# Kernel optimization log

Measured on AMD Instinct MI355X. Metric: run time of the kernel, lower is better.

## Reference

```python
import jax, jax.numpy as jnp
import numpy as np

ALPHA_MIN = 1e-6
SN_EPS = 1e-6


def _spectral_normalize(W, u):
    # One power iteration (torch spectral_norm, n_power_iterations=1).
    v = W.T @ u
    v = v / (jnp.linalg.norm(v) + SN_EPS)
    u1 = W @ v
    u1 = u1 / (jnp.linalg.norm(u1) + SN_EPS)
    u1 = jax.lax.stop_gradient(u1)
    v = jax.lax.stop_gradient(v)
    sigma = u1 @ (W @ v)
    return W / sigma


def setup_inputs() -> dict:
    key = jax.random.key(0)
    ks = jax.random.split(key, 11)
    B, T, D, K = 32, 2048, 512, 128
    x = jax.random.normal(ks[0], (B, T, D), jnp.float32)
    dt = jax.random.uniform(ks[1], (B, T), jnp.float32)
    alpha_mod = jax.random.normal(ks[2], (B, T, K), jnp.float32)
    omega_mod = jax.random.normal(ks[3], (B, T, K), jnp.float32)
    tau_mod = jax.random.normal(ks[4], (B, T, 1), jnp.float32)
    s_real_raw = jax.random.normal(ks[5], (K,), jnp.float32)
    s_imag = jax.random.normal(ks[6], (K,), jnp.float32)
    tau_raw = jax.random.normal(ks[7], (1,), jnp.float32)
    W_orig = jax.random.normal(ks[8], (K, D), jnp.float32) * (1.0 / np.sqrt(D))
    b = jax.random.normal(ks[9], (K,), jnp.float32) * 0.01
    u_sn = jax.random.normal(ks[10], (K,), jnp.float32)
    u_sn = u_sn / jnp.linalg.norm(u_sn)
    return {"x": x, "dt": dt, "alpha_mod": alpha_mod, "omega_mod": omega_mod,
            "tau_mod": tau_mod, "s_real_raw": s_real_raw, "s_imag": s_imag,
            "tau_raw": tau_raw, "W_orig": W_orig, "b": b, "u_sn": u_sn}


def reference(x, dt, alpha_mod, omega_mod, tau_mod, s_real_raw, s_imag,
              tau_raw, W_orig, b, u_sn):
    B, T, D = x.shape
    K = W_orig.shape[0]

    # global timescale and poles
    tau = jax.nn.softplus(tau_raw[0]) + 1e-3
    alpha0 = (jax.nn.softplus(s_real_raw) + ALPHA_MIN) * tau  # [K]
    omega0 = s_imag * tau                                      # [K]

    # time-varying modulation (all log-scale)
    scale = jnp.exp(tau_mod)                                   # [B,T,1]
    alpha = alpha0 * jnp.exp(alpha_mod) * scale                # [B,T,K]
    omega = omega0 * jnp.exp(omega_mod) * scale                # [B,T,K]

    dt3 = dt[..., None]                                        # [B,T,1]
    rho = jnp.exp(-alpha * dt3)                                # [B,T,K]
    theta = omega * dt3
    cos_t = jnp.cos(theta)
    sin_t = jnp.sin(theta)

    # spectral-norm projection u = x @ W_sn^T + b -> [B,T,K]
    W_sn = _spectral_normalize(W_orig, u_sn)
    u = jnp.einsum('btd,kd->btk', x, W_sn) + b

    # complex recurrence: z_t = rho_t * e^{i theta_t} * z_{t-1} + u_t
    def step(carry, inp):
        c, s = carry
        rt, ct, st, ut = inp
        c_new = rt * (c * ct - s * st) + ut
        s_new = rt * (c * st + s * ct)
        return (c_new, s_new), (c_new, s_new)

    xs = (jnp.swapaxes(rho, 0, 1), jnp.swapaxes(cos_t, 0, 1),
          jnp.swapaxes(sin_t, 0, 1), jnp.swapaxes(u, 0, 1))  # [T,B,K]
    init = (jnp.zeros((B, K), u.dtype), jnp.zeros((B, K), u.dtype))
    _, (C, S) = jax.lax.scan(step, init, xs)
    C = jnp.swapaxes(C, 0, 1)  # [B,T,K]
    S = jnp.swapaxes(S, 0, 1)
    return jnp.concatenate([C, S], axis=-1)  # [B,T,2K]
```

## Files before the change

kernel.cpp:

```cpp
#include <hip/hip_runtime.h>
#include <hip/hip_bf16.h>
#include <math.h>

typedef __bf16 bf16x8 __attribute__((ext_vector_type(8)));
typedef __bf16 bf16x4 __attribute__((ext_vector_type(4)));
typedef __bf16 bf16x2 __attribute__((ext_vector_type(2)));
typedef float f32x4 __attribute__((ext_vector_type(4)));

#define B_SZ 32
#define T_SZ 2048
#define D_SZ 512
#define K_SZ 128
#define TC 32
#define NC 64

__device__ __forceinline__ float softplus_f(float x){
  return x > 20.f ? x : log1pf(expf(x));
}

__global__ __launch_bounds__(512) void sn_prep(const float* __restrict__ W,
                                               const float* __restrict__ u_sn,
                                               __bf16* __restrict__ Wb){
  __shared__ float red[512];
  __shared__ float vsh[512];
  __shared__ float ush[128];
  const int t = threadIdx.x;
  if (t < 128) ush[t] = u_sn[t];
  __syncthreads();
  float t1 = 0.f;
  #pragma unroll 8
  for (int k = 0; k < K_SZ; ++k) t1 += W[k*D_SZ + t] * ush[k];
  red[t] = t1 * t1;
  __syncthreads();
  for (int s = 256; s > 0; s >>= 1){ if (t < s) red[t] += red[t+s]; __syncthreads(); }
  const float n1 = sqrtf(red[0]);
  vsh[t] = t1 / (n1 + 1e-6f);
  __syncthreads();
  float t2 = 0.f;
  if (t < 128){
    const float4* Wr = (const float4*)(W + (size_t)t * D_SZ);
    const float4* vp = (const float4*)vsh;
    #pragma unroll 8
    for (int d = 0; d < D_SZ/4; ++d){
      const float4 a = Wr[d], v = vp[d];
      t2 += a.x*v.x + a.y*v.y + a.z*v.z + a.w*v.w;
    }
  }
  __syncthreads();
  red[t] = (t < 128) ? t2*t2 : 0.f;
  __syncthreads();
  for (int s = 256; s > 0; s >>= 1){ if (t < s) red[t] += red[t+s]; __syncthreads(); }
  const float n2sq = red[0];
  const float sigma = n2sq / (sqrtf(n2sq) + 1e-6f);
  const float inv = 1.f / sigma;
  for (int i = t; i < K_SZ*D_SZ/4; i += 512){
    const float4 v = ((const float4*)W)[i];
    bf16x4 o; o[0]=(__bf16)(v.x*inv); o[1]=(__bf16)(v.y*inv);
    o[2]=(__bf16)(v.z*inv); o[3]=(__bf16)(v.w*inv);
    ((bf16x4*)Wb)[i] = o;
  }
}

__global__ __launch_bounds__(256) void gemm_xw(const float* __restrict__ X,
                                               const __bf16* __restrict__ Wb,
                                               __bf16* __restrict__ U){
  __shared__ bf16x8 As[2][1024];
  __shared__ bf16x8 Bs[2][1024];
  const int tid = threadIdx.x;
  const int lane = tid & 63;
  const int wid = tid >> 6;
  const int wm = wid >> 1, wn = wid & 1;
  const int rowbase = blockIdx.x * 128;
  const int L15 = lane & 15, Lq = lane >> 4;
  f32x4 acc[4][4] = {};

  const int rowA = tid >> 3;
  const int cg   = tid & 7;
  const int colo = cg * 8;
  int pidx[4];
  #pragma unroll
  for (int r = 0; r < 4; ++r){
    const int row = rowA + 32*r;
    const int fb = ((row >> 4) << 1) | (cg >> 2);
    const int ll = (row & 15) | ((cg & 3) << 4);
    pidx[r] = (fb*64 + ll) ^ cg;
  }
  const float* Xb  = X  + (size_t)(rowbase + rowA)*D_SZ + colo;
  const __bf16* Bb = Wb + (size_t)rowA*D_SZ + colo;

  float4 va[4], vb[4];
  bf16x8 wreg[4];
  #pragma unroll
  for (int r = 0; r < 4; ++r){
    const float4* q = (const float4*)(Xb + (size_t)(32*r)*D_SZ);
    va[r] = q[0]; vb[r] = q[1];
    wreg[r] = *(const bf16x8*)(Bb + (size_t)(32*r)*D_SZ);
  }

  int pb = 0;
  for (int kk = 0; kk < D_SZ; kk += 64){
    #pragma unroll
    for (int r = 0; r < 4; ++r){
      bf16x8 f;
      f[0]=(__bf16)va[r].x; f[1]=(__bf16)va[r].y; f[2]=(__bf16)va[r].z; f[3]=(__bf16)va[r].w;
      f[4]=(__bf16)vb[r].x; f[5]=(__bf16)vb[r].y; f[6]=(__bf16)vb[r].z; f[7]=(__bf16)vb[r].w;
      As[pb][pidx[r]] = f;
      Bs[pb][pidx[r]] = wreg[r];
    }
    __syncthreads();
    if (kk + 64 < D_SZ){
      #pragma unroll
      for (int r = 0; r < 4; ++r){
        const float4* q = (const float4*)(Xb + (size_t)(32*r)*D_SZ + kk + 64);
        va[r] = q[0]; vb[r] = q[1];
        wreg[r] = *(const bf16x8*)(Bb + (size_t)(32*r)*D_SZ + kk + 64);
      }
    }
    #pragma unroll
    for (int s = 0; s < 2; ++s){
      bf16x8 af[4], bfr[4];
      const int swz = (s << 2) | (lane >> 4);
      #pragma unroll
      for (int ii = 0; ii < 4; ++ii){
        const int fb = ((wm*4+ii) << 1) | s;
        af[ii] = As[pb][(fb*64 + lane) ^ swz];
      }
      #pragma unroll
      for (int jj = 0; jj < 4; ++jj){
        const int fb = ((wn*4+jj) << 1) | s;
        bfr[jj] = Bs[pb][(fb*64 + lane) ^ swz];
      }
      #pragma unroll
      for (int ii = 0; ii < 4; ++ii)
        #pragma unroll
        for (int jj = 0; jj < 4; ++jj)
          acc[ii][jj] = __builtin_amdgcn_mfma_f32_16x16x32_bf16(af[ii], bfr[jj], acc[ii][jj], 0, 0, 0);
    }
    pb ^= 1;
  }
  #pragma unroll
  for (int ii = 0; ii < 4; ++ii){
    const int m = rowbase + (wm*4+ii)*16 + (Lq << 2);
    #pragma unroll
    for (int jj = 0; jj < 4; ++jj){
      const int n = (wn*4+jj)*16 + L15;
      #pragma unroll
      for (int r = 0; r < 4; ++r)
        U[(size_t)(m + r)*K_SZ + n] = (__bf16)acc[ii][jj][r];
    }
  }
}

__global__ __launch_bounds__(256) void pass_a(
    const float* __restrict__ alpha_mod, const float* __restrict__ omega_mod,
    const __bf16* __restrict__ Uarr, const float* __restrict__ dt,
    const float* __restrict__ tau_mod, const float* __restrict__ s_real,
    const float* __restrict__ s_imag, const float* __restrict__ tau_raw,
    const float* __restrict__ bvec,
    float2* __restrict__ sumA, float2* __restrict__ sumT,
    float2* __restrict__ Zr, float2* __restrict__ Zi){
  const int t = threadIdx.x;
  const int kh = t & 63;
  const int cl = t >> 6;
  const int b = blockIdx.y;
  const int c = blockIdx.x*4 + cl;
  const int t0 = c * TC;
  __shared__ float sdt[4*TC], ssc[4*TC];
  if (t < 128){
    const int tg = blockIdx.x*4*TC + t;
    sdt[t] = dt[b*T_SZ + tg];
    ssc[t] = __expf(tau_mod[b*T_SZ + tg]);
  }
  __syncthreads();
  const float tau = softplus_f(tau_raw[0]) + 1e-3f;
  const float2 sr = ((const float2*)s_real)[kh];
  const float2 si = ((const float2*)s_imag)[kh];
  const float2 bk = ((const float2*)bvec)[kh];
  const float a0[2] = {(softplus_f(sr.x)+1e-6f)*tau, (softplus_f(sr.y)+1e-6f)*tau};
  const float w0[2] = {si.x*tau, si.y*tau};
  float zr[2]={0,0}, zs[2]={0,0}, sA[2]={0,0}, sT[2]={0,0};
  const float* sd = sdt + cl*TC;
  const float* ss = ssc + cl*TC;
  const size_t row = (size_t)(b*T_SZ + t0);
  const float2* amp = (const float2*)(alpha_mod + row*K_SZ) + kh;
  const float2* omp = (const float2*)(omega_mod + row*K_SZ) + kh;
  const bf16x2* up  = (const bf16x2*)(Uarr + row*K_SZ) + kh;
  #pragma unroll 4
  for (int i = 0; i < TC; ++i){
    const float2 am = amp[(size_t)i*64];
    const float2 om = omp[(size_t)i*64];
    const bf16x2 u2 = up[(size_t)i*64];
    const float scdt = ss[i] * sd[i];
    #pragma unroll
    for (int j = 0; j < 2; ++j){
      const float ad = a0[j] * __expf(j ? am.y : am.x) * scdt;
      const float th = w0[j] * __expf(j ? om.y : om.x) * scdt;
      const float rho = __expf(-ad);
      float st, ct; __sincosf(th, &st, &ct);
      const float uu = (float)u2[j] + (j ? bk.y : bk.x);
      const float nr = rho*(zr[j]*ct - zs[j]*st) + uu;
      const float ns = rho*(zr[j]*st + zs[j]*ct);
      zr[j] = nr; zs[j] = ns;
      sA[j] += ad; sT[j] += th;
    }
  }
  const size_t idx = ((size_t)(b*NC + c))*64 + kh;
  sumA[idx] = make_float2(sA[0], sA[1]);
  sumT[idx] = make_float2(sT[0], sT[1]);
  Zr[idx]   = make_float2(zr[0], zr[1]);
  Zi[idx]   = make_float2(zs[0], zs[1]);
}

__global__ __launch_bounds__(256) void pass_b(
    const float2* __restrict__ sumA, const float2* __restrict__ sumT,
    const float2* __restrict__ Zr, const float2* __restrict__ Zi,
    float2* __restrict__ Cr, float2* __restrict__ Ci){
  const int id = blockIdx.x*256 + threadIdx.x;
  const int b = id >> 6, kh = id & 63;
  float er[2]={0,0}, ei[2]={0,0};
  #pragma unroll 4
  for (int c = 0; c < NC; ++c){
    const size_t idx = ((size_t)(b*NC + c))*64 + kh;
    Cr[idx] = make_float2(er[0], er[1]);
    Ci[idx] = make_float2(ei[0], ei[1]);
    const float2 sa = sumA[idx], st4 = sumT[idx];
    const float2 zr = Zr[idx],   zi  = Zi[idx];
    #pragma unroll
    for (int j = 0; j < 2; ++j){
      const float rho = __expf(-(j ? sa.y : sa.x));
      float st, ct; __sincosf(j ? st4.y : st4.x, &st, &ct);
      const float ar = rho*ct, ai = rho*st;
      const float zrj = j ? zr.y : zr.x, zij = j ? zi.y : zi.x;
      const float nr = zrj + ar*er[j] - ai*ei[j];
      const float ni = zij + ar*ei[j] + ai*er[j];
      er[j] = nr; ei[j] = ni;
    }
  }
}

__global__ __launch_bounds__(256) void pass_c(
    const float* __restrict__ alpha_mod, const float* __restrict__ omega_mod,
    const __bf16* __restrict__ Uarr, const float* __restrict__ dt,
    const float* __restrict__ tau_mod, const float* __restrict__ s_real,
    const float* __restrict__ s_imag, const float* __restrict__ tau_raw,
    const float* __restrict__ bvec,
    const float2* __restrict__ Cr, const float2* __restrict__ Ci,
    float* __restrict__ out){
  const int t = threadIdx.x;
  const int kh = t & 63;
  const int cl = t >> 6;
  const int b = blockIdx.y;
  const int c = blockIdx.x*4 + cl;
  const int t0 = c * TC;
  __shared__ float sdt[4*TC], ssc[4*TC];
  if (t < 128){
    const int tg = blockIdx.x*4*TC + t;
    sdt[t] = dt[b*T_SZ + tg];
    ssc[t] = __expf(tau_mod[b*T_SZ + tg]);
  }
  __syncthreads();
  const float tau = softplus_f(tau_raw[0]) + 1e-3f;
  const float2 sr = ((const float2*)s_real)[kh];
  const float2 si = ((const float2*)s_imag)[kh];
  const float2 bk = ((const float2*)bvec)[kh];
  const float a0[2] = {(softplus_f(sr.x)+1e-6f)*tau, (softplus_f(sr.y)+1e-6f)*tau};
  const float w0[2] = {si.x*tau, si.y*tau};
  const size_t cidx = ((size_t)(b*NC + c))*64 + kh;
  const float2 cr = Cr[cidx], cim = Ci[cidx];
  float zr[2] = {cr.x, cr.y}, zs[2] = {cim.x, cim.y};
  const float* sd = sdt + cl*TC;
  const float* ss = ssc + cl*TC;
  const size_t row = (size_t)(b*T_SZ + t0);
  const float2* amp = (const float2*)(alpha_mod + row*K_SZ) + kh;
  const float2* omp = (const float2*)(omega_mod + row*K_SZ) + kh;
  const bf16x2* up  = (const bf16x2*)(Uarr + row*K_SZ) + kh;
  float2* outC = (float2*)(out + row*(2*K_SZ)) + kh;
  float2* outS = outC + 64;
  #pragma unroll 4
  for (int i = 0; i < TC; ++i){
    const float2 am = amp[(size_t)i*64];
    const float2 om = omp[(size_t)i*64];
    const bf16x2 u2 = up[(size_t)i*64];
    const float scdt = ss[i] * sd[i];
    #pragma unroll
    for (int j = 0; j < 2; ++j){
      const float ad = a0[j] * __expf(j ? am.y : am.x) * scdt;
      const float th = w0[j] * __expf(j ? om.y : om.x) * scdt;
      const float rho = __expf(-ad);
      float st, ct; __sincosf(th, &st, &ct);
      const float uu = (float)u2[j] + (j ? bk.y : bk.x);
      const float nr = rho*(zr[j]*ct - zs[j]*st) + uu;
      const float ns = rho*(zr[j]*st + zs[j]*ct);
      zr[j] = nr; zs[j] = ns;
    }
    outC[(size_t)i*128] = make_float2(zr[0], zr[1]);
    outS[(size_t)i*128] = make_float2(zs[0], zs[1]);
  }
}

extern "C" void kernel_launch(void* const* d_in, const int* in_sizes, int n_in,
                              void* d_out, int out_size, void* d_ws, size_t ws_size,
                              hipStream_t stream){
  (void)in_sizes; (void)n_in; (void)out_size; (void)ws_size;
  const float* x         = (const float*)d_in[0];
  const float* dt        = (const float*)d_in[1];
  const float* alpha_mod = (const float*)d_in[2];
  const float* omega_mod = (const float*)d_in[3];
  const float* tau_mod   = (const float*)d_in[4];
  const float* s_real    = (const float*)d_in[5];
  const float* s_imag    = (const float*)d_in[6];
  const float* tau_raw   = (const float*)d_in[7];
  const float* W         = (const float*)d_in[8];
  const float* bvec      = (const float*)d_in[9];
  const float* u_sn      = (const float*)d_in[10];
  float* out = (float*)d_out;

  char* w = (char*)d_ws;
  __bf16* Wb = (__bf16*)w;
  __bf16* U  = (__bf16*)(w + 131072);
  size_t off = 131072 + (size_t)B_SZ*T_SZ*K_SZ*2;
  const size_t SUMN = (size_t)B_SZ*NC*K_SZ*4;
  float2* sumA = (float2*)(w + off); off += SUMN;
  float2* sumT = (float2*)(w + off); off += SUMN;
  float2* Zr   = (float2*)(w + off); off += SUMN;
  float2* Zi   = (float2*)(w + off); off += SUMN;
  float2* Cr   = (float2*)(w + off); off += SUMN;
  float2* Ci   = (float2*)(w + off); off += SUMN;

  sn_prep<<<1, 512, 0, stream>>>(W, u_sn, Wb);
  gemm_xw<<<(B_SZ*T_SZ)/128, 256, 0, stream>>>(x, Wb, U);
  pass_a<<<dim3(NC/4, B_SZ), 256, 0, stream>>>(alpha_mod, omega_mod, U, dt, tau_mod,
                                               s_real, s_imag, tau_raw, bvec,
                                               sumA, sumT, Zr, Zi);
  pass_b<<<8, 256, 0, stream>>>(sumA, sumT, Zr, Zi, Cr, Ci);
  pass_c<<<dim3(NC/4, B_SZ), 256, 0, stream>>>(alpha_mod, omega_mod, U, dt, tau_mod,
                                               s_real, s_imag, tau_raw, bvec,
                                               Cr, Ci, out);
}
```

Before: 333.8 us.

## Parallelize chunk-carry scan with wave shuffles and split spectral-norm scaling kernel

The serial per-(batch,channel) loop over 64 chunks in pass_b becomes a Kogge-Stone complex affine scan across a 64-lane wave using shuffles, with one wave per (batch, channel) and many more blocks. The spectral-norm prep is split so that a single block computes only 1/sigma and a separate 64-block kernel scales W into bf16. This removes two single-block or low-parallelism serial stages that sat on the critical path. The cost is one extra launch and an extra 1/sigma workspace value, and the log-depth scan changes floating-point summation order.

```diff
diff --git a/kernel.cpp b/kernel.cpp
--- a/kernel.cpp
+++ b/kernel.cpp
@@ -18,9 +18,9 @@
   return x > 20.f ? x : log1pf(expf(x));
 }
 
-__global__ __launch_bounds__(512) void sn_prep(const float* __restrict__ W,
-                                               const float* __restrict__ u_sn,
-                                               __bf16* __restrict__ Wb){
+__global__ __launch_bounds__(512) void sn_pi(const float* __restrict__ W,
+                                             const float* __restrict__ u_sn,
+                                             float* __restrict__ sig_inv){
   __shared__ float red[512];
   __shared__ float vsh[512];
   __shared__ float ush[128];
@@ -50,15 +50,22 @@
   red[t] = (t < 128) ? t2*t2 : 0.f;
   __syncthreads();
   for (int s = 256; s > 0; s >>= 1){ if (t < s) red[t] += red[t+s]; __syncthreads(); }
-  const float n2sq = red[0];
-  const float sigma = n2sq / (sqrtf(n2sq) + 1e-6f);
-  const float inv = 1.f / sigma;
-  for (int i = t; i < K_SZ*D_SZ/4; i += 512){
-    const float4 v = ((const float4*)W)[i];
-    bf16x4 o; o[0]=(__bf16)(v.x*inv); o[1]=(__bf16)(v.y*inv);
-    o[2]=(__bf16)(v.z*inv); o[3]=(__bf16)(v.w*inv);
-    ((bf16x4*)Wb)[i] = o;
-  }
+  if (t == 0){
+    const float n2sq = red[0];
+    const float sigma = n2sq / (sqrtf(n2sq) + 1e-6f);
+    sig_inv[0] = 1.f / sigma;
+  }
+}
+
+__global__ __launch_bounds__(256) void sn_scale(const float* __restrict__ W,
+                                                const float* __restrict__ sig_inv,
+                                                __bf16* __restrict__ Wb){
+  const float inv = sig_inv[0];
+  const int i = blockIdx.x*256 + threadIdx.x;
+  const float4 v = ((const float4*)W)[i];
+  bf16x4 o; o[0]=(__bf16)(v.x*inv); o[1]=(__bf16)(v.y*inv);
+  o[2]=(__bf16)(v.z*inv); o[3]=(__bf16)(v.w*inv);
+  ((bf16x4*)Wb)[i] = o;
 }
 
 __global__ __launch_bounds__(256) void gemm_xw(const float* __restrict__ X,
@@ -166,7 +173,7 @@
   const int c = blockIdx.x*4 + cl;
   const int t0 = c * TC;
   __shared__ float sdt[4*TC], ssc[4*TC];
-  if (t < 128){
+  if (t < 4*TC){
     const int tg = blockIdx.x*4*TC + t;
     sdt[t] = dt[b*T_SZ + tg];
     ssc[t] = __expf(tau_mod[b*T_SZ + tg]);
@@ -212,30 +219,37 @@
 }
 
 __global__ __launch_bounds__(256) void pass_b(
-    const float2* __restrict__ sumA, const float2* __restrict__ sumT,
-    const float2* __restrict__ Zr, const float2* __restrict__ Zi,
-    float2* __restrict__ Cr, float2* __restrict__ Ci){
-  const int id = blockIdx.x*256 + threadIdx.x;
-  const int b = id >> 6, kh = id & 63;
-  float er[2]={0,0}, ei[2]={0,0};
-  #pragma unroll 4
-  for (int c = 0; c < NC; ++c){
-    const size_t idx = ((size_t)(b*NC + c))*64 + kh;
-    Cr[idx] = make_float2(er[0], er[1]);
-    Ci[idx] = make_float2(ei[0], ei[1]);
-    const float2 sa = sumA[idx], st4 = sumT[idx];
-    const float2 zr = Zr[idx],   zi  = Zi[idx];
-    #pragma unroll
-    for (int j = 0; j < 2; ++j){
-      const float rho = __expf(-(j ? sa.y : sa.x));
-      float st, ct; __sincosf(j ? st4.y : st4.x, &st, &ct);
-      const float ar = rho*ct, ai = rho*st;
-      const float zrj = j ? zr.y : zr.x, zij = j ? zi.y : zi.x;
-      const float nr = zrj + ar*er[j] - ai*ei[j];
-      const float ni = zij + ar*ei[j] + ai*er[j];
-      er[j] = nr; ei[j] = ni;
-    }
-  }
+    const float* __restrict__ sumA, const float* __restrict__ sumT,
+    const float* __restrict__ Zr, const float* __restrict__ Zi,
+    float* __restrict__ Cr, float* __restrict__ Ci){
+  const int gwave = (blockIdx.x*256 + threadIdx.x) >> 6;
+  const int lane  = threadIdx.x & 63;
+  const int b  = gwave >> 7;
+  const int ch = gwave & 127;
+  const size_t i0 = ((size_t)(b*NC) + lane)*128 + ch;
+  const float sa = sumA[i0], th = sumT[i0];
+  const float r = __expf(-sa);
+  float s, c; __sincosf(th, &s, &c);
+  float Fr = r*c, Fi = r*s;
+  float Ur = Zr[i0], Ui = Zi[i0];
+  #pragma unroll
+  for (int d = 1; d < 64; d <<= 1){
+    const float pFr = __shfl_up(Fr, d, 64);
+    const float pFi = __shfl_up(Fi, d, 64);
+    const float pUr = __shfl_up(Ur, d, 64);
+    const float pUi = __shfl_up(Ui, d, 64);
+    if (lane >= d){
+      const float nFr = Fr*pFr - Fi*pFi;
+      const float nFi = Fr*pFi + Fi*pFr;
+      const float nUr = Fr*pUr - Fi*pUi + Ur;
+      const float nUi = Fr*pUi + Fi*pUr + Ui;
+      Fr = nFr; Fi = nFi; Ur = nUr; Ui = nUi;
+    }
+  }
+  float er = __shfl_up(Ur, 1, 64);
+  float ei = __shfl_up(Ui, 1, 64);
+  if (lane == 0){ er = 0.f; ei = 0.f; }
+  Cr[i0] = er; Ci[i0] = ei;
 }
 
 __global__ __launch_bounds__(256) void pass_c(
@@ -253,7 +267,7 @@
   const int c = blockIdx.x*4 + cl;
   const int t0 = c * TC;
   __shared__ float sdt[4*TC], ssc[4*TC];
-  if (t < 128){
+  if (t < 4*TC){
     const int tg = blockIdx.x*4*TC + t;
     sdt[t] = dt[b*T_SZ + tg];
     ssc[t] = __expf(tau_mod[b*T_SZ + tg]);
@@ -326,13 +340,17 @@
   float2* Zi   = (float2*)(w + off); off += SUMN;
   float2* Cr   = (float2*)(w + off); off += SUMN;
   float2* Ci   = (float2*)(w + off); off += SUMN;
-
-  sn_prep<<<1, 512, 0, stream>>>(W, u_sn, Wb);
+  float* sig   = (float*)(w + off);  off += 256;
+
+  sn_pi<<<1, 512, 0, stream>>>(W, u_sn, sig);
+  sn_scale<<<64, 256, 0, stream>>>(W, sig, Wb);
   gemm_xw<<<(B_SZ*T_SZ)/128, 256, 0, stream>>>(x, Wb, U);
   pass_a<<<dim3(NC/4, B_SZ), 256, 0, stream>>>(alpha_mod, omega_mod, U, dt, tau_mod,
                                                s_real, s_imag, tau_raw, bvec,
                                                sumA, sumT, Zr, Zi);
-  pass_b<<<8, 256, 0, stream>>>(sumA, sumT, Zr, Zi, Cr, Ci);
+  pass_b<<<(B_SZ*K_SZ)/4, 256, 0, stream>>>((const float*)sumA, (const float*)sumT,
+                                            (const float*)Zr, (const float*)Zi,
+                                            (float*)Cr, (float*)Ci);
   pass_c<<<dim3(NC/4, B_SZ), 256, 0, stream>>>(alpha_mod, omega_mod, U, dt, tau_mod,
                                                s_real, s_imag, tau_raw, bvec,
                                                Cr, Ci, out);
```

Result: no change. 327.7 us (-1.8%).
